# Kernel tuning notes

Measured on AMD Instinct MI355X. Metric: run time of the kernel, lower is better.

## Reference

```python
import jax, jax.numpy as jnp
import numpy as np

B, T, N = 128, 4096, 48  # batch, seq_len, num NER tags


def setup_inputs() -> dict:
    key = jax.random.key(0)
    k1, k2, k3, k4, k5 = jax.random.split(key, 5)
    return {
        "emissions": jax.random.normal(k1, (B, T, N), dtype=jnp.float32) * 0.01,
        "transitions": jax.random.normal(k2, (N, N), dtype=jnp.float32) * 0.01,
        "start": jax.random.normal(k3, (N,), dtype=jnp.float32) * 0.01,
        "end": jax.random.normal(k4, (N,), dtype=jnp.float32) * 0.01,
        "tags": jax.random.randint(k5, (B, T), 0, N, dtype=jnp.int32),
    }


def _crf_nll(emissions, transitions, start, end, tags):
    # --- forward_partition: log Z via forward algorithm (logsumexp recursion) ---
    em_t = jnp.transpose(emissions, (1, 0, 2))  # [T, B, N]
    alpha0 = start[None, :] + em_t[0]           # dp[0][j] = start(j) + emit(0, j)

    def step(alpha, em):
        # alpha: [B, N] over previous tag y_; transitions[y_, y]
        new = jax.nn.logsumexp(alpha[:, :, None] + transitions[None, :, :], axis=1) + em
        return new, None

    alpha_T, _ = jax.lax.scan(step, alpha0, em_t[1:])  # [B, N]
    log_Z = jax.nn.logsumexp(alpha_T + end[None, :], axis=-1)  # [B]

    # --- score_seq: gold-path score ---
    em_score = jnp.take_along_axis(emissions, tags[:, :, None], axis=2)[:, :, 0].sum(axis=1)
    trans_score = transitions[tags[:, :-1], tags[:, 1:]].sum(axis=1)
    score = start[tags[:, 0]] + em_score + trans_score + end[tags[:, -1]]

    return log_Z - score  # per-sequence NLL, [B]


def reference(emissions, transitions, start, end, tags):
    return _crf_nll(emissions, transitions, start, end, tags)
```

## Files before the change

kernel.cpp:

```cpp
#include <hip/hip_runtime.h>
#include <cmath>

#define BB 128
#define TT 4096
#define NN 48

typedef short bf16x8 __attribute__((ext_vector_type(8)));
typedef short bf16x4 __attribute__((ext_vector_type(4)));
typedef float f32x4 __attribute__((ext_vector_type(4)));
typedef int   i32x4 __attribute__((ext_vector_type(4)));
typedef int   i32x2 __attribute__((ext_vector_type(2)));

__device__ __forceinline__ float wave_reduce_sum(float v) {
  #pragma unroll
  for (int m = 32; m >= 1; m >>= 1) v += __shfl_xor(v, m, 64);
  return v;
}
__device__ __forceinline__ int bperm(int byteidx, int src) {
  return __builtin_amdgcn_ds_bpermute(byteidx, src);
}
__device__ __forceinline__ float lane_bcast(float x, int lane) {
  return __uint_as_float((unsigned)__builtin_amdgcn_readlane(__float_as_int(x), lane));
}
__device__ __forceinline__ int cvt_pk_bf16(float lo, float hi) {
  int r;
  asm("v_cvt_pk_bf16_f32 %0, %1, %2" : "=v"(r) : "v"(lo), "v"(hi));
  return r;
}
__device__ __forceinline__ unsigned short f2bf(float f) {
  unsigned u = __float_as_uint(f);
  unsigned r = (u + 0x7FFFu + ((u >> 16) & 1u)) >> 16;
  return (unsigned short)r;
}

template<int NC, int CL>
__global__ __launch_bounds__(64) __attribute__((amdgpu_waves_per_eu(4, 4)))
void crf_chunk_kernel(const float* __restrict__ em,
                      const float* __restrict__ trans,
                      const int* __restrict__ tags,
                      unsigned short* __restrict__ G,
                      float* __restrict__ sc_part) {
  const int blk = blockIdx.x;
  const int b = blk / NC;
  const int c = blk % NC;
  const int l = threadIdx.x;
  const int g = l >> 4;
  const int rr = l & 15;
  const int jc = (l < NN) ? l : (NN - 1);
  const float FSCALE = 1.0f / 48.0f;

  bf16x8 Af0[3];
  bf16x4 Af1[3];
  #pragma unroll
  for (int mt = 0; mt < 3; ++mt) {
    const int i = 16 * mt + rr;
    bf16x8 a0;
    bf16x4 a1;
    #pragma unroll
    for (int e = 0; e < 8; ++e) {
      int k0 = 16 * (e >> 2) + 4 * g + (e & 3);
      a0[e] = (short)f2bf(__expf(trans[k0 * NN + i]) * FSCALE);
    }
    #pragma unroll
    for (int e = 0; e < 4; ++e) {
      int k1 = 32 + 4 * g + e;
      a1[e] = (short)f2bf(__expf(trans[k1 * NN + i]) * FSCALE);
    }
    Af0[mt] = a0; Af1[mt] = a1;
  }

  i32x4 B0s[3];
  i32x2 B1s[3];
  #pragma unroll
  for (int nt = 0; nt < 3; ++nt) {
    const int col = 16 * nt + rr;
    i32x4 b0;
    i32x2 b1;
    #pragma unroll
    for (int w = 0; w < 4; ++w) {
      int r0 = 16 * (w >> 1) + 4 * g + 2 * (w & 1);
      b0[w] = ((r0 == col) ? 0x3F80 : 0) | (((r0 + 1 == col) ? 0x3F80 : 0) << 16);
    }
    #pragma unroll
    for (int w = 0; w < 2; ++w) {
      int r0 = 32 + 4 * g + 2 * w;
      b1[w] = ((r0 == col) ? 0x3F80 : 0) | (((r0 + 1 == col) ? 0x3F80 : 0) << 16);
    }
    B0s[nt] = b0; B1s[nt] = b1;
  }

  const f32x4 zq = {0.f, 0.f, 0.f, 0.f};

  const float* embr = em + (size_t)b * TT * NN + jc;
  const int t0 = c * CL + 1;
  const int wbyte = g << 4;

  float pf0 = embr[(size_t)(t0 + 0) * NN];
  float pf1 = embr[(size_t)(t0 + 1) * NN];
  float pf2 = embr[(size_t)(t0 + 2) * NN];
  float pf3 = embr[(size_t)(t0 + 3) * NN];
  float pf4 = embr[(size_t)(t0 + 4) * NN];
  float pf5 = embr[(size_t)(t0 + 5) * NN];
  float pf6 = embr[(size_t)(t0 + 6) * NN];
  float pf7 = embr[(size_t)(t0 + 7) * NN];

  #define BODY() do {                                                         \
    float wb_[12];                                                            \
    _Pragma("unroll") for (int mt = 0; mt < 3; ++mt)                          \
    _Pragma("unroll") for (int r = 0; r < 4; ++r)                             \
      wb_[mt * 4 + r] =                                                       \
          __uint_as_float((unsigned)bperm(wbyte + mt * 64 + r * 4, wi_));     \
    _Pragma("unroll") for (int nt = 0; nt < 3; ++nt) {                        \
      bf16x4 b1c_ = __builtin_bit_cast(bf16x4, B1s[nt]);                      \
      bf16x8 b0c_ = __builtin_bit_cast(bf16x8, B0s[nt]);                      \
      f32x4 a0_ = __builtin_amdgcn_mfma_f32_16x16x16bf16_1k(Af1[0], b1c_, zq, 0, 0, 0); \
      f32x4 a1_ = __builtin_amdgcn_mfma_f32_16x16x16bf16_1k(Af1[1], b1c_, zq, 0, 0, 0); \
      f32x4 a2_ = __builtin_amdgcn_mfma_f32_16x16x16bf16_1k(Af1[2], b1c_, zq, 0, 0, 0); \
      a0_ = __builtin_amdgcn_mfma_f32_16x16x32_bf16(Af0[0], b0c_, a0_, 0, 0, 0); \
      a1_ = __builtin_amdgcn_mfma_f32_16x16x32_bf16(Af0[1], b0c_, a1_, 0, 0, 0); \
      a2_ = __builtin_amdgcn_mfma_f32_16x16x32_bf16(Af0[2], b0c_, a2_, 0, 0, 0); \
      B0s[nt][0] = cvt_pk_bf16(a0_[0] * wb_[0],  a0_[1] * wb_[1]);            \
      B0s[nt][1] = cvt_pk_bf16(a0_[2] * wb_[2],  a0_[3] * wb_[3]);            \
      B0s[nt][2] = cvt_pk_bf16(a1_[0] * wb_[4],  a1_[1] * wb_[5]);            \
      B0s[nt][3] = cvt_pk_bf16(a1_[2] * wb_[6],  a1_[3] * wb_[7]);            \
      B1s[nt][0] = cvt_pk_bf16(a2_[0] * wb_[8],  a2_[1] * wb_[9]);            \
      B1s[nt][1] = cvt_pk_bf16(a2_[2] * wb_[10], a2_[3] * wb_[11]);           \
    }                                                                         \
  } while (0)

  #define STEPF(PF, NPTR) do {                                                \
    float w_ = __expf(PF);                                                    \
    PF = *(NPTR);                                                             \
    int wi_ = __float_as_int(w_);                                             \
    BODY();                                                                   \
  } while (0)

  #define STEPC(PF, NEXT_T) do {                                              \
    float w_ = __expf(PF);                                                    \
    int nxt_ = (NEXT_T) > (TT - 1) ? (TT - 1) : (NEXT_T);                     \
    PF = embr[(size_t)nxt_ * NN];                                             \
    int wi_ = __float_as_int(w_);                                             \
    BODY();                                                                   \
  } while (0)

  if (c != NC - 1) {
    const float* pref = embr + (size_t)(t0 + 8) * NN;
    #pragma unroll 1
    for (int it = 0; it < CL / 8; ++it) {
      STEPF(pf0, pref + 0 * NN);
      STEPF(pf1, pref + 1 * NN);
      STEPF(pf2, pref + 2 * NN);
      STEPF(pf3, pref + 3 * NN);
      STEPF(pf4, pref + 4 * NN);
      STEPF(pf5, pref + 5 * NN);
      STEPF(pf6, pref + 6 * NN);
      STEPF(pf7, pref + 7 * NN);
      pref += 8 * NN;
    }
  } else {
    const float* pref = embr + (size_t)(t0 + 8) * NN;
    #pragma unroll 1
    for (int it = 0; it < CL / 8 - 2; ++it) {
      STEPF(pf0, pref + 0 * NN);
      STEPF(pf1, pref + 1 * NN);
      STEPF(pf2, pref + 2 * NN);
      STEPF(pf3, pref + 3 * NN);
      STEPF(pf4, pref + 4 * NN);
      STEPF(pf5, pref + 5 * NN);
      STEPF(pf6, pref + 6 * NN);
      STEPF(pf7, pref + 7 * NN);
      pref += 8 * NN;
    }
    const int tb = t0 + CL - 16;
    STEPC(pf0, tb + 8);
    STEPC(pf1, tb + 9);
    STEPC(pf2, tb + 10);
    STEPC(pf3, tb + 11);
    STEPC(pf4, tb + 12);
    STEPC(pf5, tb + 13);
    STEPC(pf6, tb + 14);
    STEPC(pf7, tb + 15);
    STEPC(pf0, tb + 16);
    STEPC(pf1, tb + 17);
    STEPC(pf2, tb + 18);
    STEPC(pf3, tb + 19);
    STEPC(pf4, tb + 20);
    STEPC(pf5, tb + 21);
    STEPC(pf6, tb + 22);
  }
  #undef STEPF
  #undef STEPC
  #undef BODY

  unsigned short* Gc = G + (size_t)blk * (NN * NN);
  #pragma unroll
  for (int nt = 0; nt < 3; ++nt) {
    const int rowoff = (16 * nt + rr) * NN + 4 * g;
    i32x2 d0; d0[0] = B0s[nt][0]; d0[1] = B0s[nt][1];
    i32x2 d1; d1[0] = B0s[nt][2]; d1[1] = B0s[nt][3];
    i32x2 d2; d2[0] = B1s[nt][0]; d2[1] = B1s[nt][1];
    *(i32x2*)(Gc + rowoff)      = d0;
    *(i32x2*)(Gc + rowoff + 16) = d1;
    *(i32x2*)(Gc + rowoff + 32) = d2;
  }

  const int* tgb = tags + (size_t)b * TT;
  const float* emb = em + (size_t)b * TT * NN;
  float sc = 0.0f;
  const int base = c * (TT / NC);
  #pragma unroll
  for (int q = 0; q < TT / NC; q += 64) {
    int tt = base + q + l;
    int tg = tgb[tt];
    sc += emb[(size_t)tt * NN + tg];
    if (tt > 0) sc += trans[tgb[tt - 1] * NN + tg];
  }
  sc = wave_reduce_sum(sc);
  if (l == 0) sc_part[blk] = sc;
}

template<int NC>
__launch_bounds__(64, 1)
__global__ void crf_combine_kernel(const float* __restrict__ em,
                                   const float* __restrict__ startv,
                                   const float* __restrict__ endv,
                                   const int* __restrict__ tags,
                                   const unsigned short* __restrict__ G,
                                   const float* __restrict__ sc_part,
                                   float* __restrict__ out) {
  const int b = blockIdx.x;
  const int l = threadIdx.x;
  const int jc = (l < NN) ? l : (NN - 1);
  const float* emb = em + (size_t)b * TT * NN;
  const float FSCALE = 1.0f / 48.0f;

  float r = __expf(startv[jc] + emb[jc]);

  #pragma unroll 1
  for (int c = 0; c < NC; ++c) {
    const unsigned short* Gc = G + (size_t)(b * NC + c) * (NN * NN);
    float s0 = 0.f, s1 = 0.f, s2 = 0.f, s3 = 0.f;
    #pragma unroll
    for (int i = 0; i < NN; i += 4) {
      float g0 = __uint_as_float(((unsigned)Gc[(i + 0) * NN + jc]) << 16);
      float g1 = __uint_as_float(((unsigned)Gc[(i + 1) * NN + jc]) << 16);
      float g2 = __uint_as_float(((unsigned)Gc[(i + 2) * NN + jc]) << 16);
      float g3 = __uint_as_float(((unsigned)Gc[(i + 3) * NN + jc]) << 16);
      s0 = fmaf(lane_bcast(r, i + 0), g0, s0);
      s1 = fmaf(lane_bcast(r, i + 1), g1, s1);
      s2 = fmaf(lane_bcast(r, i + 2), g2, s2);
      s3 = fmaf(lane_bcast(r, i + 3), g3, s3);
    }
    r = (s0 + s1) + (s2 + s3);
  }

  float S = wave_reduce_sum((l < NN) ? r * __expf(endv[jc]) : 0.0f);
  float scp = wave_reduce_sum((l < NC) ? sc_part[b * NC + l] : 0.0f);

  if (l == 0) {
    const int* tgb = tags + (size_t)b * TT;
    double K = -log((double)FSCALE);
    double logZ = log((double)S) + 4095.0 * K;
    double score = (double)scp + (double)startv[tgb[0]] + (double)endv[tgb[TT - 1]];
    out[b] = (float)(logZ - score);
  }
}

extern "C" void kernel_launch(void* const* d_in, const int* in_sizes, int n_in,
                              void* d_out, int out_size, void* d_ws, size_t ws_size,
                              hipStream_t stream) {
  const float* em     = (const float*)d_in[0];
  const float* trans  = (const float*)d_in[1];
  const float* startv = (const float*)d_in[2];
  const float* endv   = (const float*)d_in[3];
  const int*   tags   = (const int*)d_in[4];
  float* out = (float*)d_out;

  const size_t need32 = (size_t)BB * 32 * NN * NN * 2 + (size_t)BB * 32 * 4;
  if (ws_size >= need32) {
    constexpr int NC = 32, CL = TT / 32;
    unsigned short* G = (unsigned short*)d_ws;
    float* sc_part = (float*)((char*)d_ws + (size_t)BB * NC * NN * NN * 2);
    hipLaunchKernelGGL((crf_chunk_kernel<NC, CL>), dim3(BB * NC), dim3(64), 0, stream,
                       em, trans, tags, G, sc_part);
    hipLaunchKernelGGL((crf_combine_kernel<NC>), dim3(BB), dim3(64), 0, stream,
                       em, startv, endv, tags, G, sc_part, out);
  } else {
    constexpr int NC = 16, CL = TT / 16;
    unsigned short* G = (unsigned short*)d_ws;
    float* sc_part = (float*)((char*)d_ws + (size_t)BB * NC * NN * NN * 2);
    hipLaunchKernelGGL((crf_chunk_kernel<NC, CL>), dim3(BB * NC), dim3(64), 0, stream,
                       em, trans, tags, G, sc_part);
    hipLaunchKernelGGL((crf_combine_kernel<NC>), dim3(BB), dim3(64), 0, stream,
                       em, startv, endv, tags, G, sc_part, out);
  }
}
```

Baseline: 123.5 us.

## Pipeline emission weight broadcast one step ahead with packed bf16 pairs

Each step's exp(emission) weights are now computed and broadcast for the next timestep while the current step's MFMAs run, using double-buffered register sets. Adjacent lanes' weights are combined via DPP swap and packed into bf16 pairs, so six ds_bpermute ops replace twelve per step, and the weights are unpacked with shifts/masks. The intent is to take the cross-lane latency off the serial recurrence critical path and halve permute traffic. In exchange the weights are rounded to bf16 and each step spends extra ALU ops on packing and unpacking.

```diff
diff --git a/kernel.cpp b/kernel.cpp
--- a/kernel.cpp
+++ b/kernel.cpp
@@ -47,6 +47,7 @@
   const int g = l >> 4;
   const int rr = l & 15;
   const int jc = (l < NN) ? l : (NN - 1);
+  const bool odd = (l & 1);
   const float FSCALE = 1.0f / 48.0f;
 
   bf16x8 Af0[3];
@@ -91,9 +92,15 @@
 
   const f32x4 zq = {0.f, 0.f, 0.f, 0.f};
 
+  const int wx0 = 16 * g;
+  const int wx1 = 16 * g + 8;
+  const int wx2 = 16 * g + 64;
+  const int wx3 = 16 * g + 72;
+  const int wx4 = 16 * g + 128;
+  const int wx5 = 16 * g + 136;
+
   const float* embr = em + (size_t)b * TT * NN + jc;
   const int t0 = c * CL + 1;
-  const int wbyte = g << 4;
 
   float pf0 = embr[(size_t)(t0 + 0) * NN];
   float pf1 = embr[(size_t)(t0 + 1) * NN];
@@ -104,12 +111,30 @@
   float pf6 = embr[(size_t)(t0 + 6) * NN];
   float pf7 = embr[(size_t)(t0 + 7) * NN];
 
-  #define BODY() do {                                                         \
-    float wb_[12];                                                            \
-    _Pragma("unroll") for (int mt = 0; mt < 3; ++mt)                          \
-    _Pragma("unroll") for (int r = 0; r < 4; ++r)                             \
-      wb_[mt * 4 + r] =                                                       \
-          __uint_as_float((unsigned)bperm(wbyte + mt * 64 + r * 4, wi_));     \
+  int wa0, wa1, wa2, wa3, wa4, wa5;
+  int wb0, wb1, wb2, wb3, wb4, wb5;
+
+  #define PACKW(WSRC, d0, d1, d2, d3, d4, d5) do {                            \
+    int wi_ = __float_as_int(WSRC);                                           \
+    int nb_ = __builtin_amdgcn_update_dpp(wi_, wi_, 0xB1, 0xF, 0xF, true);    \
+    float lo_ = odd ? __int_as_float(nb_) : (WSRC);                           \
+    float hi_ = odd ? (WSRC) : __int_as_float(nb_);                           \
+    int pk_ = cvt_pk_bf16(lo_, hi_);                                          \
+    d0 = bperm(wx0, pk_); d1 = bperm(wx1, pk_);                               \
+    d2 = bperm(wx2, pk_); d3 = bperm(wx3, pk_);                               \
+    d4 = bperm(wx4, pk_); d5 = bperm(wx5, pk_);                               \
+  } while (0)
+
+  #define STEPX(PFN, RELOAD, c0, c1, c2, c3, c4, c5, n0, n1, n2, n3, n4, n5) do { \
+    float wn_ = __expf(PFN);                                                  \
+    RELOAD;                                                                   \
+    PACKW(wn_, n0, n1, n2, n3, n4, n5);                                       \
+    float u0_ = __int_as_float(c0 << 16), u1_ = __int_as_float(c0 & 0xFFFF0000); \
+    float u2_ = __int_as_float(c1 << 16), u3_ = __int_as_float(c1 & 0xFFFF0000); \
+    float u4_ = __int_as_float(c2 << 16), u5_ = __int_as_float(c2 & 0xFFFF0000); \
+    float u6_ = __int_as_float(c3 << 16), u7_ = __int_as_float(c3 & 0xFFFF0000); \
+    float u8_ = __int_as_float(c4 << 16), u9_ = __int_as_float(c4 & 0xFFFF0000); \
+    float u10_ = __int_as_float(c5 << 16), u11_ = __int_as_float(c5 & 0xFFFF0000); \
     _Pragma("unroll") for (int nt = 0; nt < 3; ++nt) {                        \
       bf16x4 b1c_ = __builtin_bit_cast(bf16x4, B1s[nt]);                      \
       bf16x8 b0c_ = __builtin_bit_cast(bf16x8, B0s[nt]);                      \
@@ -119,78 +144,70 @@
       a0_ = __builtin_amdgcn_mfma_f32_16x16x32_bf16(Af0[0], b0c_, a0_, 0, 0, 0); \
       a1_ = __builtin_amdgcn_mfma_f32_16x16x32_bf16(Af0[1], b0c_, a1_, 0, 0, 0); \
       a2_ = __builtin_amdgcn_mfma_f32_16x16x32_bf16(Af0[2], b0c_, a2_, 0, 0, 0); \
-      B0s[nt][0] = cvt_pk_bf16(a0_[0] * wb_[0],  a0_[1] * wb_[1]);            \
-      B0s[nt][1] = cvt_pk_bf16(a0_[2] * wb_[2],  a0_[3] * wb_[3]);            \
-      B0s[nt][2] = cvt_pk_bf16(a1_[0] * wb_[4],  a1_[1] * wb_[5]);            \
-      B0s[nt][3] = cvt_pk_bf16(a1_[2] * wb_[6],  a1_[3] * wb_[7]);            \
-      B1s[nt][0] = cvt_pk_bf16(a2_[0] * wb_[8],  a2_[1] * wb_[9]);            \
-      B1s[nt][1] = cvt_pk_bf16(a2_[2] * wb_[10], a2_[3] * wb_[11]);           \
+      B0s[nt][0] = cvt_pk_bf16(a0_[0] * u0_,  a0_[1] * u1_);                  \
+      B0s[nt][1] = cvt_pk_bf16(a0_[2] * u2_,  a0_[3] * u3_);                  \
+      B0s[nt][2] = cvt_pk_bf16(a1_[0] * u4_,  a1_[1] * u5_);                  \
+      B0s[nt][3] = cvt_pk_bf16(a1_[2] * u6_,  a1_[3] * u7_);                  \
+      B1s[nt][0] = cvt_pk_bf16(a2_[0] * u8_,  a2_[1] * u9_);                  \
+      B1s[nt][1] = cvt_pk_bf16(a2_[2] * u10_, a2_[3] * u11_);                 \
     }                                                                         \
   } while (0)
 
-  #define STEPF(PF, NPTR) do {                                                \
-    float w_ = __expf(PF);                                                    \
-    PF = *(NPTR);                                                             \
-    int wi_ = __float_as_int(w_);                                             \
-    BODY();                                                                   \
-  } while (0)
-
-  #define STEPC(PF, NEXT_T) do {                                              \
-    float w_ = __expf(PF);                                                    \
-    int nxt_ = (NEXT_T) > (TT - 1) ? (TT - 1) : (NEXT_T);                     \
-    PF = embr[(size_t)nxt_ * NN];                                             \
-    int wi_ = __float_as_int(w_);                                             \
-    BODY();                                                                   \
-  } while (0)
+  #define RELC(PF, NT) PF = embr[(size_t)(((NT) > (TT - 1)) ? (TT - 1) : (NT)) * NN]
+
+  {
+    float w0_ = __expf(pf0);
+    PACKW(w0_, wa0, wa1, wa2, wa3, wa4, wa5);
+  }
 
   if (c != NC - 1) {
     const float* pref = embr + (size_t)(t0 + 8) * NN;
     #pragma unroll 1
     for (int it = 0; it < CL / 8; ++it) {
-      STEPF(pf0, pref + 0 * NN);
-      STEPF(pf1, pref + 1 * NN);
-      STEPF(pf2, pref + 2 * NN);
-      STEPF(pf3, pref + 3 * NN);
-      STEPF(pf4, pref + 4 * NN);
-      STEPF(pf5, pref + 5 * NN);
-      STEPF(pf6, pref + 6 * NN);
-      STEPF(pf7, pref + 7 * NN);
+      STEPX(pf1, (pf0 = pref[0 * NN]), wa0, wa1, wa2, wa3, wa4, wa5, wb0, wb1, wb2, wb3, wb4, wb5);
+      STEPX(pf2, (pf1 = pref[1 * NN]), wb0, wb1, wb2, wb3, wb4, wb5, wa0, wa1, wa2, wa3, wa4, wa5);
+      STEPX(pf3, (pf2 = pref[2 * NN]), wa0, wa1, wa2, wa3, wa4, wa5, wb0, wb1, wb2, wb3, wb4, wb5);
+      STEPX(pf4, (pf3 = pref[3 * NN]), wb0, wb1, wb2, wb3, wb4, wb5, wa0, wa1, wa2, wa3, wa4, wa5);
+      STEPX(pf5, (pf4 = pref[4 * NN]), wa0, wa1, wa2, wa3, wa4, wa5, wb0, wb1, wb2, wb3, wb4, wb5);
+      STEPX(pf6, (pf5 = pref[5 * NN]), wb0, wb1, wb2, wb3, wb4, wb5, wa0, wa1, wa2, wa3, wa4, wa5);
+      STEPX(pf7, (pf6 = pref[6 * NN]), wa0, wa1, wa2, wa3, wa4, wa5, wb0, wb1, wb2, wb3, wb4, wb5);
+      STEPX(pf0, (pf7 = pref[7 * NN]), wb0, wb1, wb2, wb3, wb4, wb5, wa0, wa1, wa2, wa3, wa4, wa5);
       pref += 8 * NN;
     }
   } else {
     const float* pref = embr + (size_t)(t0 + 8) * NN;
     #pragma unroll 1
     for (int it = 0; it < CL / 8 - 2; ++it) {
-      STEPF(pf0, pref + 0 * NN);
-      STEPF(pf1, pref + 1 * NN);
-      STEPF(pf2, pref + 2 * NN);
-      STEPF(pf3, pref + 3 * NN);
-      STEPF(pf4, pref + 4 * NN);
-      STEPF(pf5, pref + 5 * NN);
-      STEPF(pf6, pref + 6 * NN);
-      STEPF(pf7, pref + 7 * NN);
+      STEPX(pf1, (pf0 = pref[0 * NN]), wa0, wa1, wa2, wa3, wa4, wa5, wb0, wb1, wb2, wb3, wb4, wb5);
+      STEPX(pf2, (pf1 = pref[1 * NN]), wb0, wb1, wb2, wb3, wb4, wb5, wa0, wa1, wa2, wa3, wa4, wa5);
+      STEPX(pf3, (pf2 = pref[2 * NN]), wa0, wa1, wa2, wa3, wa4, wa5, wb0, wb1, wb2, wb3, wb4, wb5);
+      STEPX(pf4, (pf3 = pref[3 * NN]), wb0, wb1, wb2, wb3, wb4, wb5, wa0, wa1, wa2, wa3, wa4, wa5);
+      STEPX(pf5, (pf4 = pref[4 * NN]), wa0, wa1, wa2, wa3, wa4, wa5, wb0, wb1, wb2, wb3, wb4, wb5);
+      STEPX(pf6, (pf5 = pref[5 * NN]), wb0, wb1, wb2, wb3, wb4, wb5, wa0, wa1, wa2, wa3, wa4, wa5);
+      STEPX(pf7, (pf6 = pref[6 * NN]), wa0, wa1, wa2, wa3, wa4, wa5, wb0, wb1, wb2, wb3, wb4, wb5);
+      STEPX(pf0, (pf7 = pref[7 * NN]), wb0, wb1, wb2, wb3, wb4, wb5, wa0, wa1, wa2, wa3, wa4, wa5);
       pref += 8 * NN;
     }
     const int tb = t0 + CL - 16;
-    STEPC(pf0, tb + 8);
-    STEPC(pf1, tb + 9);
-    STEPC(pf2, tb + 10);
-    STEPC(pf3, tb + 11);
-    STEPC(pf4, tb + 12);
-    STEPC(pf5, tb + 13);
-    STEPC(pf6, tb + 14);
-    STEPC(pf7, tb + 15);
-    STEPC(pf0, tb + 16);
-    STEPC(pf1, tb + 17);
-    STEPC(pf2, tb + 18);
-    STEPC(pf3, tb + 19);
-    STEPC(pf4, tb + 20);
-    STEPC(pf5, tb + 21);
-    STEPC(pf6, tb + 22);
-  }
-  #undef STEPF
-  #undef STEPC
-  #undef BODY
+    STEPX(pf1, RELC(pf0, tb + 8),  wa0, wa1, wa2, wa3, wa4, wa5, wb0, wb1, wb2, wb3, wb4, wb5);
+    STEPX(pf2, RELC(pf1, tb + 9),  wb0, wb1, wb2, wb3, wb4, wb5, wa0, wa1, wa2, wa3, wa4, wa5);
+    STEPX(pf3, RELC(pf2, tb + 10), wa0, wa1, wa2, wa3, wa4, wa5, wb0, wb1, wb2, wb3, wb4, wb5);
+    STEPX(pf4, RELC(pf3, tb + 11), wb0, wb1, wb2, wb3, wb4, wb5, wa0, wa1, wa2, wa3, wa4, wa5);
+    STEPX(pf5, RELC(pf4, tb + 12), wa0, wa1, wa2, wa3, wa4, wa5, wb0, wb1, wb2, wb3, wb4, wb5);
+    STEPX(pf6, RELC(pf5, tb + 13), wb0, wb1, wb2, wb3, wb4, wb5, wa0, wa1, wa2, wa3, wa4, wa5);
+    STEPX(pf7, RELC(pf6, tb + 14), wa0, wa1, wa2, wa3, wa4, wa5, wb0, wb1, wb2, wb3, wb4, wb5);
+    STEPX(pf0, RELC(pf7, tb + 15), wb0, wb1, wb2, wb3, wb4, wb5, wa0, wa1, wa2, wa3, wa4, wa5);
+    STEPX(pf1, RELC(pf0, tb + 16), wa0, wa1, wa2, wa3, wa4, wa5, wb0, wb1, wb2, wb3, wb4, wb5);
+    STEPX(pf2, RELC(pf1, tb + 17), wb0, wb1, wb2, wb3, wb4, wb5, wa0, wa1, wa2, wa3, wa4, wa5);
+    STEPX(pf3, RELC(pf2, tb + 18), wa0, wa1, wa2, wa3, wa4, wa5, wb0, wb1, wb2, wb3, wb4, wb5);
+    STEPX(pf4, RELC(pf3, tb + 19), wb0, wb1, wb2, wb3, wb4, wb5, wa0, wa1, wa2, wa3, wa4, wa5);
+    STEPX(pf5, RELC(pf4, tb + 20), wa0, wa1, wa2, wa3, wa4, wa5, wb0, wb1, wb2, wb3, wb4, wb5);
+    STEPX(pf6, RELC(pf5, tb + 21), wb0, wb1, wb2, wb3, wb4, wb5, wa0, wa1, wa2, wa3, wa4, wa5);
+    STEPX(pf7, RELC(pf6, tb + 22), wa0, wa1, wa2, wa3, wa4, wa5, wb0, wb1, wb2, wb3, wb4, wb5);
+  }
+  #undef STEPX
+  #undef PACKW
+  #undef RELC
 
   unsigned short* Gc = G + (size_t)blk * (NN * NN);
   #pragma unroll
```

Measured after the change: 129.9 us. +5.2%, slower.
